# Optimization experiments

Measured on AMD Instinct MI355X. Metric: run time of the kernel, lower is better.

Reference implementation:

```python
import jax, jax.numpy as jnp
import numpy as np

B, D, H, NB = 16384, 1024, 256, 16

def setup_inputs() -> dict:
    key = jax.random.key(0)
    ks = jax.random.split(key, 10)
    s_d = 1.0 / np.sqrt(D)
    s_h = 1.0 / np.sqrt(H)
    return {
        "x":   jax.random.normal(ks[0], (B, D), jnp.float32),
        # switch: Linear(D,H) -> relu -> Linear(H, 3*NB)
        "Ws1": jax.random.normal(ks[1], (D, H), jnp.float32) * s_d,
        "bs1": jnp.zeros((H,), jnp.float32),
        "Ws2": jax.random.normal(ks[2], (H, 3 * NB), jnp.float32) * s_h,
        "bs2": jnp.zeros((3 * NB,), jnp.float32),
        # per-branch bottleneck FC operators: D -> H -> D
        "W1":  jax.random.normal(ks[3], (NB, D, H), jnp.float32) * s_d,
        "b1":  jnp.zeros((NB, H), jnp.float32),
        "W2":  jax.random.normal(ks[4], (NB, H, D), jnp.float32) * s_h,
        "b2":  jnp.zeros((NB, D), jnp.float32),
        # noise: uniform for gumbel, normal for reparameterized gaussian
        "u":   jax.random.uniform(ks[5], (B, NB), jnp.float32, 1e-6, 1.0 - 1e-6),
        "eps": jax.random.normal(ks[6], (B, NB), jnp.float32),
    }

def reference(x, Ws1, bs1, Ws2, bs2, W1, b1, W2, b2, u, eps):
    # switch -> control signals, reshaped to (B, 3, NB)
    ctrl = jax.nn.relu(x @ Ws1 + bs1) @ Ws2 + bs2
    ctrl = ctrl.reshape(-1, 3, NB)
    y_logits, z_mean, z_logvar = ctrl[:, 0], ctrl[:, 1], ctrl[:, 2]

    # gumbel-softmax sample (tau = 1)
    g = -jnp.log(-jnp.log(u))
    y = jax.nn.softmax(y_logits + g, axis=-1)          # soft sample (B, NB)
    y_idx = jnp.argmax(y, axis=-1)                     # hard branch per sample

    # gaussian reparameterization
    z = z_mean + jnp.exp(0.5 * z_logvar) * eps         # (B, NB)

    # per-branch bottleneck FC, z of the branch gates the bottleneck
    h = jax.nn.relu(jnp.einsum('bd,ndh->bnh', x, W1) + b1)   # (B, NB, H)
    h = h * z[:, :, None]
    o = jnp.einsum('bnh,nhd->bnd', h, W2) + b2               # (B, NB, D)

    # combine: keep only the branch selected by y_idx
    onehot = jax.nn.one_hot(y_idx, NB, dtype=x.dtype)        # (B, NB)
    out = jnp.einsum('bnd,bn->bd', o, onehot)                # (B, D)

    return (x + out, y_logits, y_idx, y, z_mean, z_logvar, z)
```

## Files before the change

kernel.cpp:

```cpp
#include <hip/hip_runtime.h>
#include <hip/hip_bf16.h>
#include <stdint.h>

#define Bn 16384
#define Dd 1024
#define Hh 256
#define NBk 16

#define O1 ((size_t)Bn*Dd)
#define O2 (O1 + (size_t)Bn*NBk)
#define O3 (O2 + (size_t)Bn)
#define O4 (O3 + (size_t)Bn*NBk)
#define O5 (O4 + (size_t)Bn*NBk)
#define O6 (O5 + (size_t)Bn*NBk)

typedef __attribute__((ext_vector_type(8))) short s16x8;
typedef __attribute__((ext_vector_type(4))) float f32x4;

#define MFMA_BF16(a,b,c) __builtin_amdgcn_mfma_f32_16x16x32_bf16((a),(b),(c),0,0,0)

__device__ __forceinline__ float blo(unsigned v){ return __uint_as_float(v << 16); }
__device__ __forceinline__ float bhi(unsigned v){ return __uint_as_float(v & 0xFFFF0000u); }
__device__ __forceinline__ unsigned short f2b(float f){
  unsigned u = __float_as_uint(f);
// ... 90 lines not shown
                                           unsigned short* __restrict__ hi,
                                           unsigned short* __restrict__ lo)
{
  const int i0 = blockIdx.x * 32, j0 = blockIdx.y * 32;
  __shared__ float T[32][33];
  const int t = threadIdx.x;
  {
    const int ii = t >> 3, jj = (t & 7) * 4;
    float4 v = *(const float4*)&in[(size_t)(i0+ii)*Hh + j0 + jj];
    T[ii][jj] = v.x; T[ii][jj+1] = v.y; T[ii][jj+2] = v.z; T[ii][jj+3] = v.w;
  }
  __syncthreads();
  {
    const int jo = t >> 3, io = (t & 7) * 4;
    ushort4 sh, sl;
    float v0 = T[io+0][jo], v1 = T[io+1][jo], v2 = T[io+2][jo], v3 = T[io+3][jo];
    unsigned short h;
    h = f2b(v0); sh.x = h; sl.x = f2b(v0 - __uint_as_float((unsigned)h << 16));
    h = f2b(v1); sh.y = h; sl.y = f2b(v1 - __uint_as_float((unsigned)h << 16));
    h = f2b(v2); sh.z = h; sl.z = f2b(v2 - __uint_as_float((unsigned)h << 16));
    h = f2b(v3); sh.w = h; sl.w = f2b(v3 - __uint_as_float((unsigned)h << 16));
    *(ushort4*)&hi[(size_t)(j0+jo)*Dd + i0 + io] = sh;
    *(ushort4*)&lo[(size_t)(j0+jo)*Dd + i0 + io] = sl;
  }
}

__global__ __launch_bounds__(256) void kT2(const float* __restrict__ Ws2, float* __restrict__ Ws2T)
{
  const int j = blockIdx.x;
  const int k = threadIdx.x;
  Ws2T[(size_t)j * Hh + k] = Ws2[(size_t)k * 48 + j];
}

__global__ __launch_bounds__(256) void kA1s(const float* __restrict__ x,
    const unsigned short* __restrict__ Whi, const unsigned short* __restrict__ Wlo,
    const float* __restrict__ bs1, float* __restrict__ A1)
{
  __shared__ __align__(16) float Xs[64*64];
  __shared__ __align__(16) unsigned short Bh[128*64];
  __shared__ __align__(16) unsigned short Bl[128*64];

  const int bid = blockIdx.x;
  const int b0 = (bid >> 1) * 64;
  const int cb = bid & 1;
  const int tid = threadIdx.x, l = tid & 63, w = tid >> 6;
  const int wr = w >> 1, wc = w & 1;

  size_t xsrc[4];
  const unsigned short *hsrc[4], *lsrc[4];
  const unsigned short* Hbase = Whi + (size_t)(cb * 128) * Dd;
  const unsigned short* Lbase = Wlo + (size_t)(cb * 128) * Dd;
  #pragma unroll
  for (int t = 0; t < 4; ++t) {
    {
      int row = (w * 4 + t) * 4 + (l >> 4);
      int ga = (l & 15) ^ (row & 7);
      xsrc[t] = (size_t)(b0 + row) * Dd + ga * 4;
    }
    {
      int row = (w * 4 + t) * 8 + (l >> 3);
      int sa = (l & 7) ^ (row & 7);
      hsrc[t] = Hbase + (size_t)row * Dd + sa * 8;
      lsrc[t] = Lbase + (size_t)row * Dd + sa * 8;
    }
  }

  f32x4 acc[2][4];
  #pragma unroll
  for (int a = 0; a < 2; ++a)
    #pragma unroll
    for (int b_ = 0; b_ < 4; ++b_)
      #pragma unroll
      for (int e = 0; e < 4; ++e) acc[a][b_][e] = 0.f;

  for (int kc = 0; kc < 16; ++kc) {
    #pragma unroll
    for (int t = 0; t < 4; ++t) {
      gload16(&x[xsrc[t] + kc * 64], (char*)Xs + (w * 4 + t) * 1024);
      gload16(hsrc[t] + kc * 64, (char*)Bh + (w * 4 + t) * 1024);
      gload16(lsrc[t] + kc * 64, (char*)Bl + (w * 4 + t) * 1024);
    }
    __syncthreads();

    #pragma unroll
    for (int kk = 0; kk < 2; ++kk) {
      s16x8 ahi[2], alo[2], bh[4], bl[4];
      #pragma unroll
      for (int rf = 0; rf < 2; ++rf) {
        const int row = wr * 32 + rf * 16 + (l & 15);
        const int gl = 8 * kk + 2 * (l >> 4);
        const int g0 = gl ^ (row & 7), g1 = (gl + 1) ^ (row & 7);
        f32x4 u0 = *(const f32x4*)((const char*)Xs + row * 256 + g0 * 16);
        f32x4 u1 = *(const f32x4*)((const char*)Xs + row * 256 + g1 * 16);
        split8(u0, u1, ahi[rf], alo[rf]);
      }
      #pragma unroll
      for (int cf = 0; cf < 4; ++cf) {
        const int col = wc * 64 + cf * 16 + (l & 15);
        const int s8 = (4 * kk + (l >> 4)) ^ (col & 7);
        bh[cf] = *(const s16x8*)((const char*)Bh + col * 128 + s8 * 16);
        bl[cf] = *(const s16x8*)((const char*)Bl + col * 128 + s8 * 16);
      }
      #pragma unroll
      for (int rf = 0; rf < 2; ++rf)
        #pragma unroll
        for (int cf = 0; cf < 4; ++cf) {
          acc[rf][cf] = MFMA_BF16(ahi[rf], bh[cf], acc[rf][cf]);
          acc[rf][cf] = MFMA_BF16(ahi[rf], bl[cf], acc[rf][cf]);
          acc[rf][cf] = MFMA_BF16(alo[rf], bh[cf], acc[rf][cf]);
        }
    }
    __syncthreads();
  }

  #pragma unroll
  for (int rf = 0; rf < 2; ++rf)
    #pragma unroll
    for (int cf = 0; cf < 4; ++cf)
      #pragma unroll
      for (int rg = 0; rg < 4; ++rg) {
        const int row = b0 + wr * 32 + rf * 16 + (l >> 4) * 4 + rg;
        const int col = cb * 128 + wc * 64 + cf * 16 + (l & 15);
        A1[(size_t)row * Hh + col] = fmaxf(acc[rf][cf][rg] + bs1[col], 0.f);
      }
}

__global__ __launch_bounds__(256) void kA2(const float* __restrict__ Ws2, const float* __restrict__ bs2,
                                           float* out)
{
  const int b0 = blockIdx.x * 64;
  __shared__ float XS[32][68];
  __shared__ float WC[32][48];
  const int tid = threadIdx.x;
  const int rg = tid >> 4, jg = tid & 15;
  float acc[4][3];
  #pragma unroll
  for (int r = 0; r < 4; ++r) { acc[r][0]=0.f; acc[r][1]=0.f; acc[r][2]=0.f; }
  const float* A1 = out;
  for (int kc = 0; kc < 8; ++kc) {
    const int k0 = kc*32;
    #pragma unroll
    for (int it = 0; it < 2; ++it) {
      int i = tid + 256*it;
      int row = i >> 3, kq = i & 7;
      float4 v = *(const float4*)&A1[(size_t)(b0+row)*Hh + k0 + 4*kq];
      XS[4*kq+0][row]=v.x; XS[4*kq+1][row]=v.y; XS[4*kq+2][row]=v.z; XS[4*kq+3][row]=v.w;
    }
    #pragma unroll
    for (int it = 0; it < 2; ++it) {
      int i = tid + 256*it;
      if (i < 384) {
        int k = i / 12, jq = i % 12;
        *(float4*)&WC[k][4*jq] = *(const float4*)&Ws2[(size_t)(k0+k)*48 + 4*jq];
      }
    }
    __syncthreads();
    #pragma unroll
// ... 287 lines not shown
        f32x4 u0 = *(const f32x4*)((const char*)Xs + row * 256 + g0 * 16);
        f32x4 u1 = *(const f32x4*)((const char*)Xs + row * 256 + g1 * 16);
        af[rf] = cvt8(u0, u1);
      }
      #pragma unroll
      for (int cf = 0; cf < 4; ++cf) {
        const int col = wc * 64 + cf * 16 + (l & 15);
        const int s8 = (4 * kk + (l >> 4)) ^ (col & 7);
        bf[cf] = *(const s16x8*)((const char*)Wsh + col * 128 + s8 * 16);
      }
      #pragma unroll
      for (int rf = 0; rf < 2; ++rf)
        #pragma unroll
        for (int cf = 0; cf < 4; ++cf)
          acc[rf][cf] = MFMA_BF16(af[rf], bf[cf], acc[rf][cf]);
    }
    __syncthreads();
  }

  const size_t hrow0 = (size_t)seg[n] + r0;
  #pragma unroll
  for (int rf = 0; rf < 2; ++rf)
    #pragma unroll
    for (int cf = 0; cf < 4; ++cf)
      #pragma unroll
      for (int rg = 0; rg < 4; ++rg) {
        const int rloc = wr * 32 + rf * 16 + (l >> 4) * 4 + rg;
        const int col = cb * 128 + wc * 64 + cf * 16 + (l & 15);
        const float hv = fmaxf(acc[rf][cf][rg] + b1[n * Hh + col], 0.f) * zrs[rloc];
        hbuf[(hrow0 + rloc) * Hh + col] = f2b(hv);
      }
}

__global__ __launch_bounds__(256) void kG2(const float* __restrict__ x,
    const unsigned short* __restrict__ W2T, const float* __restrict__ b2,
    const unsigned short* __restrict__ hbuf, const int* __restrict__ rowlist,
    const int* __restrict__ offs, const int* __restrict__ tp2, const int* __restrict__ seg,
    float* __restrict__ out)
{
  __shared__ __align__(16) unsigned short As[128*64];
  __shared__ __align__(16) unsigned short Bs[128*64];
  __shared__ int rows_s[128];

  const int bid = blockIdx.x;
  const int tile = bid >> 3, cb = bid & 7;
  if (tile >= tp2[NBk]) return;
  int n = 0;
  while (tile >= tp2[n+1]) ++n;
  const int tt = tile - tp2[n];
  const int base = offs[n], cnt = offs[n+1] - base;
  const int r0 = tt * 128;
  const int tid = threadIdx.x, l = tid & 63, w = tid >> 6;
  const int wr = w >> 1, wc = w & 1;

  if (tid < 128) {
    int r = r0 + tid;
    rows_s[tid] = rowlist[base + (r < cnt ? r : cnt - 1)];
  }
  __syncthreads();

  const unsigned short* Abase = hbuf + (size_t)(seg[n] + r0) * Hh;
  const unsigned short* Bbase = W2T + (size_t)n * (Hh * Dd) + (size_t)(cb * 128) * Hh;

  const unsigned short* asrc[4];
  const unsigned short* bsrc[4];
  #pragma unroll
// ... 28 lines not shown
        const int row = wr * 64 + rf * 16 + (l & 15);
        const int s8 = (4 * kk + (l >> 4)) ^ (row & 7);
        af[rf] = *(const s16x8*)((const char*)As + row * 128 + s8 * 16);
      }
      #pragma unroll
      for (int cf = 0; cf < 4; ++cf) {
        const int col = wc * 64 + cf * 16 + (l & 15);
        const int s8 = (4 * kk + (l >> 4)) ^ (col & 7);
        bf[cf] = *(const s16x8*)((const char*)Bs + col * 128 + s8 * 16);
      }
      #pragma unroll
      for (int rf = 0; rf < 4; ++rf)
        #pragma unroll
        for (int cf = 0; cf < 4; ++cf)
          acc[rf][cf] = MFMA_BF16(af[rf], bf[cf], acc[rf][cf]);
    }
    __syncthreads();
  }

  #pragma unroll
  for (int rf = 0; rf < 4; ++rf)
    #pragma unroll
    for (int rg = 0; rg < 4; ++rg) {
      const int rloc = wr * 64 + rf * 16 + (l >> 4) * 4 + rg;
      if (r0 + rloc < cnt) {
        const int g = rows_s[rloc];
        #pragma unroll
        for (int cf = 0; cf < 4; ++cf) {
          const int col = cb * 128 + wc * 64 + cf * 16 + (l & 15);
          out[(size_t)g * Dd + col] = acc[rf][cf][rg] + b2[n * Dd + col] + x[(size_t)g * Dd + col];
        }
      }
    }
}

__global__ __launch_bounds__(256) void kCm(const float* __restrict__ x,
    const unsigned short* __restrict__ W1T, const float* __restrict__ b1,
    const unsigned short* __restrict__ W2T, const float* __restrict__ b2,
    const int* __restrict__ rowlist, const float* __restrict__ zsel,
    const int* __restrict__ offs, float* __restrict__ out)
{
  __shared__ __align__(16) char LDSA[55808];
  char* HSp  = LDSA;
  char* XSp  = LDSA + 33792;
  char* W1Sp = LDSA + 33792 + 4096;
  char* W2Sp = LDSA + 33792;
  float* b1s = (float*)(LDSA + 54272);
  int*   rows = (int*)(LDSA + 55296);
  float* zrs  = (float*)(LDSA + 55552);

  const int tid = threadIdx.x;
  const int l = tid & 63, w = tid >> 6;
  const int xcd = blockIdx.x & 7, slot0 = blockIdx.x >> 3;
  const int n0 = 2 * xcd;
  const int oA = offs[n0], oB = offs[n0+1], oC = offs[n0+2];
  const int cA = oB - oA, cB = oC - oB;
  const int nb0 = (cA + 63) >> 6, nb1 = (cB + 63) >> 6;

  const int sr = tid >> 2, sq = tid & 3;

  for (int si = slot0; si < nb0 + nb1; si += 64) {
    int n, base, cnt, tt;
    if (si < nb0) { n = n0;     tt = si;        base = oA; cnt = cA; }
    else          { n = n0 + 1; tt = si - nb0;  base = oB; cnt = cB; }
    const int r0 = tt * 64;

    __syncthreads();
    if (tid < 64) {
      int r = r0 + tid;
      int g = rowlist[base + (r < cnt ? r : cnt - 1)];
      rows[tid] = g;
      zrs[tid]  = zsel[g];
    }
    b1s[tid] = b1[n * Hh + tid];
    __syncthreads();

    const size_t xrow = (size_t)rows[sr] * Dd;
    const size_t w1o = (size_t)n * (Dd * Hh);
    const size_t w2o = (size_t)n * (Hh * Dd);

    f32x4 acc1[4][4];
    #pragma unroll
    for (int a = 0; a < 4; ++a)
      #pragma unroll
      for (int b_ = 0; b_ < 4; ++b_)
        #pragma unroll
        for (int e = 0; e < 4; ++e) acc1[a][b_][e] = 0.f;

    const int arow  = (l & 15) * 64 + (l >> 4) * 16;
    const int brow1 = w * 4096 + (l & 15) * 64 + (l >> 4) * 16;

    float4 xa, xb; uint4 wv0, wv1, wv2, wv3;
    xa = *(const float4*)&x[xrow + sq * 8];
    xb = *(const float4*)&x[xrow + sq * 8 + 4];
    wv0 = *(const uint4*)&W1T[w1o + (size_t)(  0 + sr) * Dd + sq * 8];
    wv1 = *(const uint4*)&W1T[w1o + (size_t)( 64 + sr) * Dd + sq * 8];
    wv2 = *(const uint4*)&W1T[w1o + (size_t)(128 + sr) * Dd + sq * 8];
    wv3 = *(const uint4*)&W1T[w1o + (size_t)(192 + sr) * Dd + sq * 8];
    {
      s16x8 xs;
      xs[0]=(short)f2b(xa.x); xs[1]=(short)f2b(xa.y); xs[2]=(short)f2b(xa.z); xs[3]=(short)f2b(xa.w);
      xs[4]=(short)f2b(xb.x); xs[5]=(short)f2b(xb.y); xs[6]=(short)f2b(xb.z); xs[7]=(short)f2b(xb.w);
      *(s16x8*)(XSp + 16 * tid) = xs;
      *(uint4*)(W1Sp +     0 + 16 * tid) = wv0;
      *(uint4*)(W1Sp +  4096 + 16 * tid) = wv1;
      *(uint4*)(W1Sp +  8192 + 16 * tid) = wv2;
      *(uint4*)(W1Sp + 12288 + 16 * tid) = wv3;
    }
    __syncthreads();

    for (int kc = 0; kc < 32; ++kc) {
      const bool more = kc < 31;
      if (more) {
        const int ko = (kc + 1) * 32 + sq * 8;
        xa = *(const float4*)&x[xrow + ko];
        xb = *(const float4*)&x[xrow + ko + 4];
        wv0 = *(const uint4*)&W1T[w1o + (size_t)(  0 + sr) * Dd + ko];
        wv1 = *(const uint4*)&W1T[w1o + (size_t)( 64 + sr) * Dd + ko];
        wv2 = *(const uint4*)&W1T[w1o + (size_t)(128 + sr) * Dd + ko];
        wv3 = *(const uint4*)&W1T[w1o + (size_t)(192 + sr) * Dd + ko];
      }
      s16x8 af[4], bf[4];
      #pragma unroll
      for (int rt = 0; rt < 4; ++rt) af[rt] = *(const s16x8*)(XSp + rt * 1024 + arow);
      #pragma unroll
      for (int ct = 0; ct < 4; ++ct) bf[ct] = *(const s16x8*)(W1Sp + brow1 + ct * 1024);
      #pragma unroll
      for (int rt = 0; rt < 4; ++rt)
        #pragma unroll
        for (int ct = 0; ct < 4; ++ct)
          acc1[rt][ct] = MFMA_BF16(af[rt], bf[ct], acc1[rt][ct]);
      __syncthreads();
      if (more) {
        s16x8 xs;
        xs[0]=(short)f2b(xa.x); xs[1]=(short)f2b(xa.y); xs[2]=(short)f2b(xa.z); xs[3]=(short)f2b(xa.w);
        xs[4]=(short)f2b(xb.x); xs[5]=(short)f2b(xb.y); xs[6]=(short)f2b(xb.z); xs[7]=(short)f2b(xb.w);
        *(s16x8*)(XSp + 16 * tid) = xs;
        *(uint4*)(W1Sp +     0 + 16 * tid) = wv0;
        *(uint4*)(W1Sp +  4096 + 16 * tid) = wv1;
        *(uint4*)(W1Sp +  8192 + 16 * tid) = wv2;
        *(uint4*)(W1Sp + 12288 + 16 * tid) = wv3;
      }
      __syncthreads();
    }

    #pragma unroll
    for (int rt = 0; rt < 4; ++rt)
      #pragma unroll
      for (int ct = 0; ct < 4; ++ct)
        #pragma unroll
        for (int rg = 0; rg < 4; ++rg) {
          const int row = rt * 16 + 4 * (l >> 4) + rg;
          const int col = w * 64 + ct * 16 + (l & 15);
          const float hv = fmaxf(acc1[rt][ct][rg] + b1s[col], 0.f) * zrs[row];
          *(unsigned short*)(HSp + row * 528 + col * 2) = f2b(hv);
        }
    __syncthreads();

    uint4 v0, v1, v2, v3;
    v0 = *(const uint4*)&W2T[w2o + (size_t)(  0 + sr) * Hh + sq * 8];
    v1 = *(const uint4*)&W2T[w2o + (size_t)( 64 + sr) * Hh + sq * 8];
    v2 = *(const uint4*)&W2T[w2o + (size_t)(128 + sr) * Hh + sq * 8];
    v3 = *(const uint4*)&W2T[w2o + (size_t)(192 + sr) * Hh + sq * 8];
    *(uint4*)(W2Sp +     0 + 16 * tid) = v0;
    *(uint4*)(W2Sp +  4096 + 16 * tid) = v1;
    *(uint4*)(W2Sp +  8192 + 16 * tid) = v2;
    *(uint4*)(W2Sp + 12288 + 16 * tid) = v3;
    __syncthreads();

    for (int s = 0; s < 4; ++s) {
      f32x4 acc2[4][4];
      #pragma unroll
      for (int a = 0; a < 4; ++a)
        #pragma unroll
        for (int b_ = 0; b_ < 4; ++b_)
          #pragma unroll
          for (int e = 0; e < 4; ++e) acc2[a][b_][e] = 0.f;

      for (int kc = 0; kc < 8; ++kc) {
        int ns = s, nk = kc + 1;
        if (nk == 8) { ns = s + 1; nk = 0; }
        const bool more = ns < 4;
        if (more) {
          const size_t dbase = w2o + (size_t)(ns * 256) * Hh;
          const int ko = nk * 32 + sq * 8;
          v0 = *(const uint4*)&W2T[dbase + (size_t)(  0 + sr) * Hh + ko];
          v1 = *(const uint4*)&W2T[dbase + (size_t)( 64 + sr) * Hh + ko];
          v2 = *(const uint4*)&W2T[dbase + (size_t)(128 + sr) * Hh + ko];
          v3 = *(const uint4*)&W2T[dbase + (size_t)(192 + sr) * Hh + ko];
        }
        s16x8 af[4], bf[4];
        #pragma unroll
        for (int rt = 0; rt < 4; ++rt)
          af[rt] = *(const s16x8*)(HSp + (rt * 16 + (l & 15)) * 528 + kc * 64 + (l >> 4) * 16);
        #pragma unroll
        for (int ct = 0; ct < 4; ++ct)
          bf[ct] = *(const s16x8*)(W2Sp + (w * 64 + ct * 16 + (l & 15)) * 64 + (l >> 4) * 16);
        #pragma unroll
        for (int rt = 0; rt < 4; ++rt)
          #pragma unroll
          for (int ct = 0; ct < 4; ++ct)
            acc2[rt][ct] = MFMA_BF16(af[rt], bf[ct], acc2[rt][ct]);
        __syncthreads();
        if (more) {
          *(uint4*)(W2Sp +     0 + 16 * tid) = v0;
          *(uint4*)(W2Sp +  4096 + 16 * tid) = v1;
          *(uint4*)(W2Sp +  8192 + 16 * tid) = v2;
          *(uint4*)(W2Sp + 12288 + 16 * tid) = v3;
        }
        __syncthreads();
      }

      #pragma unroll
      for (int rt = 0; rt < 4; ++rt)
        #pragma unroll
        for (int ct = 0; ct < 4; ++ct)
          #pragma unroll
          for (int rg = 0; rg < 4; ++rg) {
            const int row = rt * 16 + 4 * (l >> 4) + rg;
            if (r0 + row < cnt) {
              const int g = rows[row];
              const int d = s * 256 + w * 64 + ct * 16 + (l & 15);
              out[(size_t)g * Dd + d] = acc2[rt][ct][rg] + b2[n * Dd + d] + x[(size_t)g * Dd + d];
            }
          }
    }
  }
}

extern "C" void kernel_launch(void* const* d_in, const int* in_sizes, int n_in,
                              void* d_out, int out_size, void* d_ws, size_t ws_size,
                              hipStream_t stream) {
  const float* x   = (const float*)d_in[0];
  const float* Ws1 = (const float*)d_in[1];
  const float* bs1 = (const float*)d_in[2];
  const float* Ws2 = (const float*)d_in[3];
  const float* bs2 = (const float*)d_in[4];
  const float* W1  = (const float*)d_in[5];
  const float* b1  = (const float*)d_in[6];
  const float* W2  = (const float*)d_in[7];
  const float* b2  = (const float*)d_in[8];
  const float* u   = (const float*)d_in[9];
  const float* eps = (const float*)d_in[10];
  float* out = (float*)d_out;

  char* ws = (char*)d_ws;
  int*   counts  = (int*)(ws + 0);
  int*   cursor  = (int*)(ws + 64);
  int*   bpre    = (int*)(ws + 128);
  int*   offs    = (int*)(ws + 256);
  int*   tp1     = (int*)(ws + 384);
  int*   tp2     = (int*)(ws + 512);
  int*   seg     = (int*)(ws + 640);
  int*   idxw    = (int*)(ws + 4096);
  float* zsel    = (float*)(ws + 4096 + 65536);
  int*   rowlist = (int*)(ws + 4096 + 131072);
  float* Ws2T    = (float*)(ws + 786432);
  unsigned short* W1T  = (unsigned short*)(ws + ((size_t)1 << 20));
  unsigned short* W2T  = (unsigned short*)(ws + ((size_t)9 << 20));
  unsigned short* hbuf = (unsigned short*)(ws + ((size_t)17 << 20));
  unsigned short* Whi  = (unsigned short*)(ws + ((size_t)27 << 20));
  unsigned short* Wlo  = (unsigned short*)(ws + ((size_t)27 << 20) + (512<<10));

  const bool f2 = ws_size >= ((size_t)28 << 20);
  const bool f1 = ws_size >= ((size_t)18 << 20);

  hipMemsetAsync(d_ws, 0, 4096, stream);
  if (f1 || f2) {
    kT<<<dim3(32, 8, 16), 256, 0, stream>>>(W1, W1T, Dd, Hh);
    kT<<<dim3(8, 32, 16), 256, 0, stream>>>(W2, W2T, Hh, Dd);
  }
  if (f2) {
    kTW<<<dim3(32, 8), 256, 0, stream>>>(Ws1, Whi, Wlo);
    kT2<<<dim3(48), 256, 0, stream>>>(Ws2, Ws2T);
    kA1s<<<dim3(512), 256, 0, stream>>>(x, Whi, Wlo, bs1, out);
    kB3<<<dim3(Bn/16), 256, 0, stream>>>(out, Ws2T, bs2, u, eps, out, idxw, zsel);
    kH <<<dim3(Bn/256), 256, 0, stream>>>(idxw, counts);
  } else {
    kA1<<<dim3(Bn/64, 2), 256, 0, stream>>>(x, Ws1, bs1, out);
    kA2<<<dim3(Bn/64), 256, 0, stream>>>(Ws2, bs2, out);
    kB2<<<dim3(Bn*NBk/256), 256, 0, stream>>>(u, eps, out, idxw, zsel, counts);
  }
  kP <<<dim3(1), 64, 0, stream>>>(counts, offs, cursor, bpre, tp1, tp2, seg);
  if (f2) {
    kS2<<<dim3(Bn/256), 256, 0, stream>>>(idxw, cursor, rowlist);
    kG1<<<dim3(544), 256, 0, stream>>>(x, W1T, b1, rowlist, zsel, offs, tp1, seg, hbuf);
    kG2<<<dim3(1152), 256, 0, stream>>>(x, W2T, b2, hbuf, rowlist, offs, tp2, seg, out);
  } else {
    kS<<<dim3(Bn/256), 256, 0, stream>>>(idxw, cursor, rowlist);
    if (f1)
      kCm<<<dim3(512), 256, 0, stream>>>(x, W1T, b1, W2T, b2, rowlist, zsel, offs, out);
  }
}
```

Measured before the change: 159.7 us.

## Pre-split x into bf16 hi/lo once and reuse in switch and branch GEMMs

Adds a pass that converts x into bf16 high and low halves in workspace. A new switch GEMM kernel reads these directly through async global-to-LDS loads with swizzled layout and smaller 64x64 tiles. A new first branch GEMM reads the bf16 high part instead of fp32 x. This is meant to remove repeated fp32-to-bf16 conversion and halve x traffic inside both GEMMs, at the cost of an extra 64MB write plus reads and a 92MB workspace requirement. The unused fused kCm fallback is removed, so the smallest workspace path no longer computes the branch output.

```diff
diff --git a/kernel.cpp b/kernel.cpp
--- a/kernel.cpp
+++ b/kernel.cpp
@@ -146,6 +146,19 @@
   Ws2T[(size_t)j * Hh + k] = Ws2[(size_t)k * 48 + j];
 }
 
+__global__ __launch_bounds__(256) void kTX(const float* __restrict__ x,
+                                           unsigned short* __restrict__ xh,
+                                           unsigned short* __restrict__ xl)
+{
+  const size_t i = ((size_t)blockIdx.x * 256 + threadIdx.x) * 8;
+  const f32x4 u0 = *(const f32x4*)&x[i];
+  const f32x4 u1 = *(const f32x4*)&x[i + 4];
+  s16x8 hi, lo;
+  split8(u0, u1, hi, lo);
+  *(s16x8*)&xh[i] = hi;
+  *(s16x8*)&xl[i] = lo;
+}
+
 __global__ __launch_bounds__(256) void kA1s(const float* __restrict__ x,
     const unsigned short* __restrict__ Whi, const unsigned short* __restrict__ Wlo,
     const float* __restrict__ bs1, float* __restrict__ A1)
@@ -237,6 +250,86 @@
         const int col = cb * 128 + wc * 64 + cf * 16 + (l & 15);
         A1[(size_t)row * Hh + col] = fmaxf(acc[rf][cf][rg] + bs1[col], 0.f);
       }
+}
+
+__global__ __launch_bounds__(256) void kA1s2(const unsigned short* __restrict__ Xhi,
+    const unsigned short* __restrict__ Xlo,
+    const unsigned short* __restrict__ Whi, const unsigned short* __restrict__ Wlo,
+    const float* __restrict__ bs1, float* __restrict__ A1)
+{
+  __shared__ __align__(16) unsigned short Xh[64*64];
+  __shared__ __align__(16) unsigned short Xl[64*64];
+  __shared__ __align__(16) unsigned short Bh[64*64];
+  __shared__ __align__(16) unsigned short Bl[64*64];
+
+  const int bid = blockIdx.x;
+  const int b0 = (bid >> 2) * 64;
+  const int cb = bid & 3;
+  const int tid = threadIdx.x, l = tid & 63, w = tid >> 6;
+
+  const unsigned short *xhs[2], *xls[2], *whs[2], *wls[2];
+  int ldst[2];
+  const unsigned short* Hbase = Whi + (size_t)(cb * 64) * Dd;
+  const unsigned short* Lbase = Wlo + (size_t)(cb * 64) * Dd;
+  #pragma unroll
+  for (int t = 0; t < 2; ++t) {
+    const int row = (w * 2 + t) * 8 + (l >> 3);
+    const int sa = (l & 7) ^ (row & 7);
+    xhs[t] = Xhi + (size_t)(b0 + row) * Dd + sa * 8;
+    xls[t] = Xlo + (size_t)(b0 + row) * Dd + sa * 8;
+    whs[t] = Hbase + (size_t)row * Dd + sa * 8;
+    wls[t] = Lbase + (size_t)row * Dd + sa * 8;
+    ldst[t] = (w * 2 + t) * 1024;
+  }
+
+  f32x4 acc[4];
+  #pragma unroll
+  for (int cf = 0; cf < 4; ++cf)
+    #pragma unroll
+    for (int e = 0; e < 4; ++e) acc[cf][e] = 0.f;
+
+  for (int kc = 0; kc < 16; ++kc) {
+    #pragma unroll
+    for (int t = 0; t < 2; ++t) {
+      gload16(xhs[t] + kc * 64, (char*)Xh + ldst[t]);
+      gload16(xls[t] + kc * 64, (char*)Xl + ldst[t]);
+      gload16(whs[t] + kc * 64, (char*)Bh + ldst[t]);
+      gload16(wls[t] + kc * 64, (char*)Bl + ldst[t]);
+    }
+    __syncthreads();
+
+    #pragma unroll
+    for (int kk = 0; kk < 2; ++kk) {
+      const int arow = w * 16 + (l & 15);
+      const int as8 = (4 * kk + (l >> 4)) ^ (arow & 7);
+      const s16x8 ah = *(const s16x8*)((const char*)Xh + arow * 128 + as8 * 16);
+      const s16x8 al = *(const s16x8*)((const char*)Xl + arow * 128 + as8 * 16);
+      s16x8 bh[4], bl[4];
+      #pragma unroll
+      for (int cf = 0; cf < 4; ++cf) {
+        const int col = cf * 16 + (l & 15);
+        const int s8 = (4 * kk + (l >> 4)) ^ (col & 7);
+        bh[cf] = *(const s16x8*)((const char*)Bh + col * 128 + s8 * 16);
+        bl[cf] = *(const s16x8*)((const char*)Bl + col * 128 + s8 * 16);
+      }
+      #pragma unroll
+      for (int cf = 0; cf < 4; ++cf) {
+        acc[cf] = MFMA_BF16(ah, bh[cf], acc[cf]);
+        acc[cf] = MFMA_BF16(ah, bl[cf], acc[cf]);
+        acc[cf] = MFMA_BF16(al, bh[cf], acc[cf]);
+      }
+    }
+    __syncthreads();
+  }
+
+  #pragma unroll
+  for (int cf = 0; cf < 4; ++cf)
+    #pragma unroll
+    for (int rg = 0; rg < 4; ++rg) {
+      const int row = b0 + w * 16 + (l >> 4) * 4 + rg;
+      const int col = cb * 64 + cf * 16 + (l & 15);
+      A1[(size_t)row * Hh + col] = fmaxf(acc[cf][rg] + bs1[col], 0.f);
+    }
 }
 
 __global__ __launch_bounds__(256) void kA2(const float* __restrict__ Ws2, const float* __restrict__ bs2,
@@ -590,6 +683,109 @@
       }
 }
 
+__global__ __launch_bounds__(256) void kG1b(const unsigned short* __restrict__ Xhi,
+    const unsigned short* __restrict__ W1T, const float* __restrict__ b1,
+    const int* __restrict__ rowlist, const float* __restrict__ zsel,
+    const int* __restrict__ offs, const int* __restrict__ tp1, const int* __restrict__ seg,
+    unsigned short* __restrict__ hbuf)
+{
+  __shared__ __align__(16) unsigned short Xsh[64*64];
+  __shared__ __align__(16) unsigned short Wsh[128*64];
+  __shared__ int rows_s[64];
+  __shared__ float zrs[64];
+
+  const int bid = blockIdx.x;
+  const int tile = bid >> 1, cb = bid & 1;
+  if (tile >= tp1[NBk]) return;
+  int n = 0;
+  while (tile >= tp1[n+1]) ++n;
+  const int tt = tile - tp1[n];
+  const int base = offs[n], cnt = offs[n+1] - base;
+  const int r0 = tt * 64;
+  const int tid = threadIdx.x, l = tid & 63, w = tid >> 6;
+  const int wr = w >> 1, wc = w & 1;
+
+  if (tid < 64) {
+    int r = r0 + tid;
+    int g = rowlist[base + (r < cnt ? r : cnt - 1)];
+    rows_s[tid] = g;
+    zrs[tid] = zsel[g];
+  }
+  __syncthreads();
+
+  const unsigned short* xsrc[2];
+  int xdst[2];
+  const unsigned short* wsrc[4];
+  const unsigned short* Wbase = W1T + (size_t)n * (Hh * Dd) + (size_t)(cb * 128) * Dd;
+  #pragma unroll
+  for (int t = 0; t < 2; ++t) {
+    const int row = (w * 2 + t) * 8 + (l >> 3);
+    const int sa = (l & 7) ^ (row & 7);
+    xsrc[t] = Xhi + (size_t)rows_s[row] * Dd + sa * 8;
+    xdst[t] = (w * 2 + t) * 1024;
+  }
+  #pragma unroll
+  for (int t = 0; t < 4; ++t) {
+    const int row = (w * 4 + t) * 8 + (l >> 3);
+    const int sa = (l & 7) ^ (row & 7);
+    wsrc[t] = Wbase + (size_t)row * Dd + sa * 8;
+  }
+
+  f32x4 acc[2][4];
+  #pragma unroll
+  for (int a = 0; a < 2; ++a)
+    #pragma unroll
+    for (int b_ = 0; b_ < 4; ++b_)
+      #pragma unroll
+      for (int e = 0; e < 4; ++e) acc[a][b_][e] = 0.f;
+
+  for (int kc = 0; kc < 16; ++kc) {
+    #pragma unroll
+    for (int t = 0; t < 2; ++t)
+      gload16(xsrc[t] + kc * 64, (char*)Xsh + xdst[t]);
+    #pragma unroll
+    for (int t = 0; t < 4; ++t)
+      gload16(wsrc[t] + kc * 64, (char*)Wsh + (w * 4 + t) * 1024);
+    __syncthreads();
+
+    #pragma unroll
+    for (int kk = 0; kk < 2; ++kk) {
+      s16x8 af[2], bf[4];
+      #pragma unroll
+      for (int rf = 0; rf < 2; ++rf) {
+        const int row = wr * 32 + rf * 16 + (l & 15);
+        const int s8 = (4 * kk + (l >> 4)) ^ (row & 7);
+        af[rf] = *(const s16x8*)((const char*)Xsh + row * 128 + s8 * 16);
+      }
+      #pragma unroll
+      for (int cf = 0; cf < 4; ++cf) {
+        const int col = wc * 64 + cf * 16 + (l & 15);
+        const int s8 = (4 * kk + (l >> 4)) ^ (col & 7);
+        bf[cf] = *(const s16x8*)((const char*)Wsh + col * 128 + s8 * 16);
+      }
+      #pragma unroll
+      for (int rf = 0; rf < 2; ++rf)
+        #pragma unroll
+        for (int cf = 0; cf < 4; ++cf)
+          acc[rf][cf] = MFMA_BF16(af[rf], bf[cf], acc[rf][cf]);
+    }
+    __syncthreads();
+  }
+
+  const size_t hrow0 = (size_t)seg[n] + r0;
+  #pragma unroll
+  for (int rf = 0; rf < 2; ++rf)
+    #pragma unroll
+    for (int cf = 0; cf < 4; ++cf)
+      #pragma unroll
+      for (int rg = 0; rg < 4; ++rg) {
+        const int rloc = wr * 32 + rf * 16 + (l >> 4) * 4 + rg;
+        const int col = cb * 128 + wc * 64 + cf * 16 + (l & 15);
+        const float hv = fmaxf(acc[rf][cf][rg] + b1[n * Hh + col], 0.f) * zrs[rloc];
+        hbuf[(hrow0 + rloc) * Hh + col] = f2b(hv);
+      }
+}
+
 __global__ __launch_bounds__(256) void kG2(const float* __restrict__ x,
     const unsigned short* __restrict__ W2T, const float* __restrict__ b2,
     const unsigned short* __restrict__ hbuf, const int* __restrict__ rowlist,
@@ -684,200 +880,6 @@
         }
       }
     }
-}
-
-__global__ __launch_bounds__(256) void kCm(const float* __restrict__ x,
-    const unsigned short* __restrict__ W1T, const float* __restrict__ b1,
-    const unsigned short* __restrict__ W2T, const float* __restrict__ b2,
-    const int* __restrict__ rowlist, const float* __restrict__ zsel,
-    const int* __restrict__ offs, float* __restrict__ out)
-{
-  __shared__ __align__(16) char LDSA[55808];
-  char* HSp  = LDSA;
-  char* XSp  = LDSA + 33792;
-  char* W1Sp = LDSA + 33792 + 4096;
-  char* W2Sp = LDSA + 33792;
-  float* b1s = (float*)(LDSA + 54272);
-  int*   rows = (int*)(LDSA + 55296);
-  float* zrs  = (float*)(LDSA + 55552);
-
-  const int tid = threadIdx.x;
-  const int l = tid & 63, w = tid >> 6;
-  const int xcd = blockIdx.x & 7, slot0 = blockIdx.x >> 3;
-  const int n0 = 2 * xcd;
-  const int oA = offs[n0], oB = offs[n0+1], oC = offs[n0+2];
-  const int cA = oB - oA, cB = oC - oB;
-  const int nb0 = (cA + 63) >> 6, nb1 = (cB + 63) >> 6;
-
-  const int sr = tid >> 2, sq = tid & 3;
-
-  for (int si = slot0; si < nb0 + nb1; si += 64) {
-    int n, base, cnt, tt;
-    if (si < nb0) { n = n0;     tt = si;        base = oA; cnt = cA; }
-    else          { n = n0 + 1; tt = si - nb0;  base = oB; cnt = cB; }
-    const int r0 = tt * 64;
-
-    __syncthreads();
-    if (tid < 64) {
-      int r = r0 + tid;
-      int g = rowlist[base + (r < cnt ? r : cnt - 1)];
-      rows[tid] = g;
-      zrs[tid]  = zsel[g];
-    }
-    b1s[tid] = b1[n * Hh + tid];
-    __syncthreads();
-
-    const size_t xrow = (size_t)rows[sr] * Dd;
-    const size_t w1o = (size_t)n * (Dd * Hh);
-    const size_t w2o = (size_t)n * (Hh * Dd);
-
-    f32x4 acc1[4][4];
-    #pragma unroll
-    for (int a = 0; a < 4; ++a)
-      #pragma unroll
-      for (int b_ = 0; b_ < 4; ++b_)
-        #pragma unroll
-        for (int e = 0; e < 4; ++e) acc1[a][b_][e] = 0.f;
-
-    const int arow  = (l & 15) * 64 + (l >> 4) * 16;
-    const int brow1 = w * 4096 + (l & 15) * 64 + (l >> 4) * 16;
-
-    float4 xa, xb; uint4 wv0, wv1, wv2, wv3;
-    xa = *(const float4*)&x[xrow + sq * 8];
-    xb = *(const float4*)&x[xrow + sq * 8 + 4];
-    wv0 = *(const uint4*)&W1T[w1o + (size_t)(  0 + sr) * Dd + sq * 8];
-    wv1 = *(const uint4*)&W1T[w1o + (size_t)( 64 + sr) * Dd + sq * 8];
-    wv2 = *(const uint4*)&W1T[w1o + (size_t)(128 + sr) * Dd + sq * 8];
-    wv3 = *(const uint4*)&W1T[w1o + (size_t)(192 + sr) * Dd + sq * 8];
-    {
-      s16x8 xs;
-      xs[0]=(short)f2b(xa.x); xs[1]=(short)f2b(xa.y); xs[2]=(short)f2b(xa.z); xs[3]=(short)f2b(xa.w);
-      xs[4]=(short)f2b(xb.x); xs[5]=(short)f2b(xb.y); xs[6]=(short)f2b(xb.z); xs[7]=(short)f2b(xb.w);
-      *(s16x8*)(XSp + 16 * tid) = xs;
-      *(uint4*)(W1Sp +     0 + 16 * tid) = wv0;
-      *(uint4*)(W1Sp +  4096 + 16 * tid) = wv1;
-      *(uint4*)(W1Sp +  8192 + 16 * tid) = wv2;
-      *(uint4*)(W1Sp + 12288 + 16 * tid) = wv3;
-    }
-    __syncthreads();
-
-    for (int kc = 0; kc < 32; ++kc) {
-      const bool more = kc < 31;
-      if (more) {
-        const int ko = (kc + 1) * 32 + sq * 8;
-        xa = *(const float4*)&x[xrow + ko];
-        xb = *(const float4*)&x[xrow + ko + 4];
-        wv0 = *(const uint4*)&W1T[w1o + (size_t)(  0 + sr) * Dd + ko];
-        wv1 = *(const uint4*)&W1T[w1o + (size_t)( 64 + sr) * Dd + ko];
-        wv2 = *(const uint4*)&W1T[w1o + (size_t)(128 + sr) * Dd + ko];
-        wv3 = *(const uint4*)&W1T[w1o + (size_t)(192 + sr) * Dd + ko];
-      }
-      s16x8 af[4], bf[4];
-      #pragma unroll
-      for (int rt = 0; rt < 4; ++rt) af[rt] = *(const s16x8*)(XSp + rt * 1024 + arow);
-      #pragma unroll
-      for (int ct = 0; ct < 4; ++ct) bf[ct] = *(const s16x8*)(W1Sp + brow1 + ct * 1024);
-      #pragma unroll
-      for (int rt = 0; rt < 4; ++rt)
-        #pragma unroll
-        for (int ct = 0; ct < 4; ++ct)
-          acc1[rt][ct] = MFMA_BF16(af[rt], bf[ct], acc1[rt][ct]);
-      __syncthreads();
-      if (more) {
-        s16x8 xs;
-        xs[0]=(short)f2b(xa.x); xs[1]=(short)f2b(xa.y); xs[2]=(short)f2b(xa.z); xs[3]=(short)f2b(xa.w);
-        xs[4]=(short)f2b(xb.x); xs[5]=(short)f2b(xb.y); xs[6]=(short)f2b(xb.z); xs[7]=(short)f2b(xb.w);
-        *(s16x8*)(XSp + 16 * tid) = xs;
-        *(uint4*)(W1Sp +     0 + 16 * tid) = wv0;
-        *(uint4*)(W1Sp +  4096 + 16 * tid) = wv1;
-        *(uint4*)(W1Sp +  8192 + 16 * tid) = wv2;
-        *(uint4*)(W1Sp + 12288 + 16 * tid) = wv3;
-      }
-      __syncthreads();
-    }
-
-    #pragma unroll
-    for (int rt = 0; rt < 4; ++rt)
-      #pragma unroll
-      for (int ct = 0; ct < 4; ++ct)
-        #pragma unroll
-        for (int rg = 0; rg < 4; ++rg) {
-          const int row = rt * 16 + 4 * (l >> 4) + rg;
-          const int col = w * 64 + ct * 16 + (l & 15);
-          const float hv = fmaxf(acc1[rt][ct][rg] + b1s[col], 0.f) * zrs[row];
-          *(unsigned short*)(HSp + row * 528 + col * 2) = f2b(hv);
-        }
-    __syncthreads();
-
-    uint4 v0, v1, v2, v3;
-    v0 = *(const uint4*)&W2T[w2o + (size_t)(  0 + sr) * Hh + sq * 8];
-    v1 = *(const uint4*)&W2T[w2o + (size_t)( 64 + sr) * Hh + sq * 8];
-    v2 = *(const uint4*)&W2T[w2o + (size_t)(128 + sr) * Hh + sq * 8];
-    v3 = *(const uint4*)&W2T[w2o + (size_t)(192 + sr) * Hh + sq * 8];
-    *(uint4*)(W2Sp +     0 + 16 * tid) = v0;
-    *(uint4*)(W2Sp +  4096 + 16 * tid) = v1;
-    *(uint4*)(W2Sp +  8192 + 16 * tid) = v2;
-    *(uint4*)(W2Sp + 12288 + 16 * tid) = v3;
-    __syncthreads();
-
-    for (int s = 0; s < 4; ++s) {
-      f32x4 acc2[4][4];
-      #pragma unroll
-      for (int a = 0; a < 4; ++a)
-        #pragma unroll
-        for (int b_ = 0; b_ < 4; ++b_)
-          #pragma unroll
-          for (int e = 0; e < 4; ++e) acc2[a][b_][e] = 0.f;
-
-      for (int kc = 0; kc < 8; ++kc) {
-        int ns = s, nk = kc + 1;
-        if (nk == 8) { ns = s + 1; nk = 0; }
-        const bool more = ns < 4;
-        if (more) {
-          const size_t dbase = w2o + (size_t)(ns * 256) * Hh;
-          const int ko = nk * 32 + sq * 8;
-          v0 = *(const uint4*)&W2T[dbase + (size_t)(  0 + sr) * Hh + ko];
-          v1 = *(const uint4*)&W2T[dbase + (size_t)( 64 + sr) * Hh + ko];
-          v2 = *(const uint4*)&W2T[dbase + (size_t)(128 + sr) * Hh + ko];
-          v3 = *(const uint4*)&W2T[dbase + (size_t)(192 + sr) * Hh + ko];
-        }
-        s16x8 af[4], bf[4];
-        #pragma unroll
-        for (int rt = 0; rt < 4; ++rt)
-          af[rt] = *(const s16x8*)(HSp + (rt * 16 + (l & 15)) * 528 + kc * 64 + (l >> 4) * 16);
-        #pragma unroll
-        for (int ct = 0; ct < 4; ++ct)
-          bf[ct] = *(const s16x8*)(W2Sp + (w * 64 + ct * 16 + (l & 15)) * 64 + (l >> 4) * 16);
-        #pragma unroll
-        for (int rt = 0; rt < 4; ++rt)
-          #pragma unroll
-          for (int ct = 0; ct < 4; ++ct)
-            acc2[rt][ct] = MFMA_BF16(af[rt], bf[ct], acc2[rt][ct]);
-        __syncthreads();
-        if (more) {
-          *(uint4*)(W2Sp +     0 + 16 * tid) = v0;
-          *(uint4*)(W2Sp +  4096 + 16 * tid) = v1;
-          *(uint4*)(W2Sp +  8192 + 16 * tid) = v2;
-          *(uint4*)(W2Sp + 12288 + 16 * tid) = v3;
-        }
-        __syncthreads();
-      }
-
-      #pragma unroll
-      for (int rt = 0; rt < 4; ++rt)
-        #pragma unroll
-        for (int ct = 0; ct < 4; ++ct)
-          #pragma unroll
-          for (int rg = 0; rg < 4; ++rg) {
-            const int row = rt * 16 + 4 * (l >> 4) + rg;
-            if (r0 + row < cnt) {
-              const int g = rows[row];
-              const int d = s * 256 + w * 64 + ct * 16 + (l & 15);
-              out[(size_t)g * Dd + d] = acc2[rt][ct][rg] + b2[n * Dd + d] + x[(size_t)g * Dd + d];
-            }
-          }
-    }
-  }
 }
 
 extern "C" void kernel_launch(void* const* d_in, const int* in_sizes, int n_in,
@@ -913,7 +915,10 @@
   unsigned short* hbuf = (unsigned short*)(ws + ((size_t)17 << 20));
   unsigned short* Whi  = (unsigned short*)(ws + ((size_t)27 << 20));
   unsigned short* Wlo  = (unsigned short*)(ws + ((size_t)27 << 20) + (512<<10));
-
+  unsigned short* Xhi  = (unsigned short*)(ws + ((size_t)28 << 20));
+  unsigned short* Xlo  = (unsigned short*)(ws + ((size_t)60 << 20));
+
+  const bool f3 = ws_size >= ((size_t)92 << 20);
   const bool f2 = ws_size >= ((size_t)28 << 20);
   const bool f1 = ws_size >= ((size_t)18 << 20);
 
@@ -925,7 +930,12 @@
   if (f2) {
     kTW<<<dim3(32, 8), 256, 0, stream>>>(Ws1, Whi, Wlo);
     kT2<<<dim3(48), 256, 0, stream>>>(Ws2, Ws2T);
-    kA1s<<<dim3(512), 256, 0, stream>>>(x, Whi, Wlo, bs1, out);
+    if (f3) {
+      kTX<<<dim3(Bn*Dd/2048), 256, 0, stream>>>(x, Xhi, Xlo);
+      kA1s2<<<dim3(1024), 256, 0, stream>>>(Xhi, Xlo, Whi, Wlo, bs1, out);
+    } else {
+      kA1s<<<dim3(512), 256, 0, stream>>>(x, Whi, Wlo, bs1, out);
+    }
     kB3<<<dim3(Bn/16), 256, 0, stream>>>(out, Ws2T, bs2, u, eps, out, idxw, zsel);
     kH <<<dim3(Bn/256), 256, 0, stream>>>(idxw, counts);
   } else {
@@ -936,11 +946,12 @@
   kP <<<dim3(1), 64, 0, stream>>>(counts, offs, cursor, bpre, tp1, tp2, seg);
   if (f2) {
     kS2<<<dim3(Bn/256), 256, 0, stream>>>(idxw, cursor, rowlist);
-    kG1<<<dim3(544), 256, 0, stream>>>(x, W1T, b1, rowlist, zsel, offs, tp1, seg, hbuf);
+    if (f3)
+      kG1b<<<dim3(544), 256, 0, stream>>>(Xhi, W1T, b1, rowlist, zsel, offs, tp1, seg, hbuf);
+    else
+      kG1<<<dim3(544), 256, 0, stream>>>(x, W1T, b1, rowlist, zsel, offs, tp1, seg, hbuf);
     kG2<<<dim3(1152), 256, 0, stream>>>(x, W2T, b2, hbuf, rowlist, offs, tp2, seg, out);
   } else {
     kS<<<dim3(Bn/256), 256, 0, stream>>>(idxw, cursor, rowlist);
-    if (f1)
-      kCm<<<dim3(512), 256, 0, stream>>>(x, W1T, b1, W2T, b2, rowlist, zsel, offs, out);
-  }
-}
+  }
+}
```

New measurement: 173.5 us. 1.09x slower.

## Split x into bf16 hi/lo once per tile in first switch GEMM, halve row tile

Applied to the files above, without the earlier changes.

The first switch GEMM kernel now converts each x element to bf16 hi/lo once when it is staged into shared memory, and stores it as bf16. Before, every wave re-split fp32 tiles on each fragment read. The row tile drops from 64 to 32 rows, each wave covers 32 columns instead of a 2x4 fragment grid, and the grid doubles to 1024 blocks. The x load for the next k-chunk is register-prefetched while MFMAs run on the current chunk. The unused fallback kernel kCm is removed, so the small-workspace path no longer computes the branch output, though that path does not run normally.

```diff
diff --git a/kernel.cpp b/kernel.cpp
--- a/kernel.cpp
+++ b/kernel.cpp
@@ -146,82 +146,89 @@
   Ws2T[(size_t)j * Hh + k] = Ws2[(size_t)k * 48 + j];
 }
 
-__global__ __launch_bounds__(256) void kA1s(const float* __restrict__ x,
+__global__ __launch_bounds__(256) void kA1s3(const float* __restrict__ x,
     const unsigned short* __restrict__ Whi, const unsigned short* __restrict__ Wlo,
     const float* __restrict__ bs1, float* __restrict__ A1)
 {
-  __shared__ __align__(16) float Xs[64*64];
+  __shared__ __align__(16) unsigned short Xh[32*64];
+  __shared__ __align__(16) unsigned short Xl[32*64];
   __shared__ __align__(16) unsigned short Bh[128*64];
   __shared__ __align__(16) unsigned short Bl[128*64];
 
   const int bid = blockIdx.x;
-  const int b0 = (bid >> 1) * 64;
+  const int b0 = (bid >> 1) * 32;
   const int cb = bid & 1;
   const int tid = threadIdx.x, l = tid & 63, w = tid >> 6;
-  const int wr = w >> 1, wc = w & 1;
-
-  size_t xsrc[4];
+
+  const int xrow = tid >> 3, xga = tid & 7;
+  const int xdst = xrow * 128 + (xga ^ (xrow & 7)) * 16;
+  const size_t xsrc = (size_t)(b0 + xrow) * Dd + xga * 8;
+
   const unsigned short *hsrc[4], *lsrc[4];
   const unsigned short* Hbase = Whi + (size_t)(cb * 128) * Dd;
   const unsigned short* Lbase = Wlo + (size_t)(cb * 128) * Dd;
   #pragma unroll
   for (int t = 0; t < 4; ++t) {
-    {
-      int row = (w * 4 + t) * 4 + (l >> 4);
-      int ga = (l & 15) ^ (row & 7);
-      xsrc[t] = (size_t)(b0 + row) * Dd + ga * 4;
-    }
-    {
-      int row = (w * 4 + t) * 8 + (l >> 3);
-      int sa = (l & 7) ^ (row & 7);
-      hsrc[t] = Hbase + (size_t)row * Dd + sa * 8;
-      lsrc[t] = Lbase + (size_t)row * Dd + sa * 8;
-    }
-  }
-
-  f32x4 acc[2][4];
+    const int col = (w * 4 + t) * 8 + (l >> 3);
+    const int sa = (l & 7) ^ (col & 7);
+    hsrc[t] = Hbase + (size_t)col * Dd + sa * 8;
+    lsrc[t] = Lbase + (size_t)col * Dd + sa * 8;
+  }
+
+  f32x4 acc[2][2];
   #pragma unroll
   for (int a = 0; a < 2; ++a)
     #pragma unroll
-    for (int b_ = 0; b_ < 4; ++b_)
+    for (int b_ = 0; b_ < 2; ++b_)
       #pragma unroll
       for (int e = 0; e < 4; ++e) acc[a][b_][e] = 0.f;
 
+  f32x4 xa = *(const f32x4*)&x[xsrc];
+  f32x4 xb = *(const f32x4*)&x[xsrc + 4];
+
   for (int kc = 0; kc < 16; ++kc) {
     #pragma unroll
     for (int t = 0; t < 4; ++t) {
-      gload16(&x[xsrc[t] + kc * 64], (char*)Xs + (w * 4 + t) * 1024);
       gload16(hsrc[t] + kc * 64, (char*)Bh + (w * 4 + t) * 1024);
       gload16(lsrc[t] + kc * 64, (char*)Bl + (w * 4 + t) * 1024);
     }
-    __syncthreads();
+    {
+      s16x8 hi8, lo8;
+      split8(xa, xb, hi8, lo8);
+      *(s16x8*)((char*)Xh + xdst) = hi8;
+      *(s16x8*)((char*)Xl + xdst) = lo8;
+    }
+    __syncthreads();
+
+    if (kc < 15) {
+      xa = *(const f32x4*)&x[xsrc + (kc + 1) * 64];
+      xb = *(const f32x4*)&x[xsrc + (kc + 1) * 64 + 4];
+    }
 
     #pragma unroll
     for (int kk = 0; kk < 2; ++kk) {
-      s16x8 ahi[2], alo[2], bh[4], bl[4];
+      s16x8 ah[2], al[2], bh[2], bl[2];
       #pragma unroll
       for (int rf = 0; rf < 2; ++rf) {
-        const int row = wr * 32 + rf * 16 + (l & 15);
-        const int gl = 8 * kk + 2 * (l >> 4);
-        const int g0 = gl ^ (row & 7), g1 = (gl + 1) ^ (row & 7);
-        f32x4 u0 = *(const f32x4*)((const char*)Xs + row * 256 + g0 * 16);
-        f32x4 u1 = *(const f32x4*)((const char*)Xs + row * 256 + g1 * 16);
-        split8(u0, u1, ahi[rf], alo[rf]);
-      }
-      #pragma unroll
-      for (int cf = 0; cf < 4; ++cf) {
-        const int col = wc * 64 + cf * 16 + (l & 15);
-        const int s8 = (4 * kk + (l >> 4)) ^ (col & 7);
-        bh[cf] = *(const s16x8*)((const char*)Bh + col * 128 + s8 * 16);
-        bl[cf] = *(const s16x8*)((const char*)Bl + col * 128 + s8 * 16);
+        const int row = rf * 16 + (l & 15);
+        const int g = (kk * 4 + (l >> 4)) ^ (row & 7);
+        ah[rf] = *(const s16x8*)((const char*)Xh + row * 128 + g * 16);
+        al[rf] = *(const s16x8*)((const char*)Xl + row * 128 + g * 16);
+      }
+      #pragma unroll
+      for (int cf = 0; cf < 2; ++cf) {
+        const int col = w * 32 + cf * 16 + (l & 15);
+        const int g = (kk * 4 + (l >> 4)) ^ (col & 7);
+        bh[cf] = *(const s16x8*)((const char*)Bh + col * 128 + g * 16);
+        bl[cf] = *(const s16x8*)((const char*)Bl + col * 128 + g * 16);
       }
       #pragma unroll
       for (int rf = 0; rf < 2; ++rf)
         #pragma unroll
-        for (int cf = 0; cf < 4; ++cf) {
-          acc[rf][cf] = MFMA_BF16(ahi[rf], bh[cf], acc[rf][cf]);
-          acc[rf][cf] = MFMA_BF16(ahi[rf], bl[cf], acc[rf][cf]);
-          acc[rf][cf] = MFMA_BF16(alo[rf], bh[cf], acc[rf][cf]);
+        for (int cf = 0; cf < 2; ++cf) {
+          acc[rf][cf] = MFMA_BF16(ah[rf], bh[cf], acc[rf][cf]);
+          acc[rf][cf] = MFMA_BF16(ah[rf], bl[cf], acc[rf][cf]);
+          acc[rf][cf] = MFMA_BF16(al[rf], bh[cf], acc[rf][cf]);
         }
     }
     __syncthreads();
@@ -230,11 +237,11 @@
   #pragma unroll
   for (int rf = 0; rf < 2; ++rf)
     #pragma unroll
-    for (int cf = 0; cf < 4; ++cf)
+    for (int cf = 0; cf < 2; ++cf)
       #pragma unroll
       for (int rg = 0; rg < 4; ++rg) {
-        const int row = b0 + wr * 32 + rf * 16 + (l >> 4) * 4 + rg;
-        const int col = cb * 128 + wc * 64 + cf * 16 + (l & 15);
+        const int row = b0 + rf * 16 + (l >> 4) * 4 + rg;
+        const int col = cb * 128 + w * 32 + cf * 16 + (l & 15);
         A1[(size_t)row * Hh + col] = fmaxf(acc[rf][cf][rg] + bs1[col], 0.f);
       }
 }
@@ -684,200 +691,6 @@
         }
       }
     }
-}
-
-__global__ __launch_bounds__(256) void kCm(const float* __restrict__ x,
-    const unsigned short* __restrict__ W1T, const float* __restrict__ b1,
-    const unsigned short* __restrict__ W2T, const float* __restrict__ b2,
-    const int* __restrict__ rowlist, const float* __restrict__ zsel,
-    const int* __restrict__ offs, float* __restrict__ out)
-{
-  __shared__ __align__(16) char LDSA[55808];
-  char* HSp  = LDSA;
-  char* XSp  = LDSA + 33792;
-  char* W1Sp = LDSA + 33792 + 4096;
-  char* W2Sp = LDSA + 33792;
-  float* b1s = (float*)(LDSA + 54272);
-  int*   rows = (int*)(LDSA + 55296);
-  float* zrs  = (float*)(LDSA + 55552);
-
-  const int tid = threadIdx.x;
-  const int l = tid & 63, w = tid >> 6;
-  const int xcd = blockIdx.x & 7, slot0 = blockIdx.x >> 3;
-  const int n0 = 2 * xcd;
-  const int oA = offs[n0], oB = offs[n0+1], oC = offs[n0+2];
-  const int cA = oB - oA, cB = oC - oB;
-  const int nb0 = (cA + 63) >> 6, nb1 = (cB + 63) >> 6;
-
-  const int sr = tid >> 2, sq = tid & 3;
-
-  for (int si = slot0; si < nb0 + nb1; si += 64) {
-    int n, base, cnt, tt;
-    if (si < nb0) { n = n0;     tt = si;        base = oA; cnt = cA; }
-    else          { n = n0 + 1; tt = si - nb0;  base = oB; cnt = cB; }
-    const int r0 = tt * 64;
-
-    __syncthreads();
-    if (tid < 64) {
-      int r = r0 + tid;
-      int g = rowlist[base + (r < cnt ? r : cnt - 1)];
-      rows[tid] = g;
-      zrs[tid]  = zsel[g];
-    }
-    b1s[tid] = b1[n * Hh + tid];
-    __syncthreads();
-
-    const size_t xrow = (size_t)rows[sr] * Dd;
-    const size_t w1o = (size_t)n * (Dd * Hh);
-    const size_t w2o = (size_t)n * (Hh * Dd);
-
-    f32x4 acc1[4][4];
-    #pragma unroll
-    for (int a = 0; a < 4; ++a)
-      #pragma unroll
-      for (int b_ = 0; b_ < 4; ++b_)
-        #pragma unroll
-        for (int e = 0; e < 4; ++e) acc1[a][b_][e] = 0.f;
-
-    const int arow  = (l & 15) * 64 + (l >> 4) * 16;
-    const int brow1 = w * 4096 + (l & 15) * 64 + (l >> 4) * 16;
-
-    float4 xa, xb; uint4 wv0, wv1, wv2, wv3;
-    xa = *(const float4*)&x[xrow + sq * 8];
-    xb = *(const float4*)&x[xrow + sq * 8 + 4];
-    wv0 = *(const uint4*)&W1T[w1o + (size_t)(  0 + sr) * Dd + sq * 8];
-    wv1 = *(const uint4*)&W1T[w1o + (size_t)( 64 + sr) * Dd + sq * 8];
-    wv2 = *(const uint4*)&W1T[w1o + (size_t)(128 + sr) * Dd + sq * 8];
-    wv3 = *(const uint4*)&W1T[w1o + (size_t)(192 + sr) * Dd + sq * 8];
-    {
-      s16x8 xs;
-      xs[0]=(short)f2b(xa.x); xs[1]=(short)f2b(xa.y); xs[2]=(short)f2b(xa.z); xs[3]=(short)f2b(xa.w);
-      xs[4]=(short)f2b(xb.x); xs[5]=(short)f2b(xb.y); xs[6]=(short)f2b(xb.z); xs[7]=(short)f2b(xb.w);
-      *(s16x8*)(XSp + 16 * tid) = xs;
-      *(uint4*)(W1Sp +     0 + 16 * tid) = wv0;
-      *(uint4*)(W1Sp +  4096 + 16 * tid) = wv1;
-      *(uint4*)(W1Sp +  8192 + 16 * tid) = wv2;
-      *(uint4*)(W1Sp + 12288 + 16 * tid) = wv3;
-    }
-    __syncthreads();
-
-    for (int kc = 0; kc < 32; ++kc) {
-      const bool more = kc < 31;
-      if (more) {
-        const int ko = (kc + 1) * 32 + sq * 8;
-        xa = *(const float4*)&x[xrow + ko];
-        xb = *(const float4*)&x[xrow + ko + 4];
-        wv0 = *(const uint4*)&W1T[w1o + (size_t)(  0 + sr) * Dd + ko];
-        wv1 = *(const uint4*)&W1T[w1o + (size_t)( 64 + sr) * Dd + ko];
-        wv2 = *(const uint4*)&W1T[w1o + (size_t)(128 + sr) * Dd + ko];
-        wv3 = *(const uint4*)&W1T[w1o + (size_t)(192 + sr) * Dd + ko];
-      }
-      s16x8 af[4], bf[4];
-      #pragma unroll
-      for (int rt = 0; rt < 4; ++rt) af[rt] = *(const s16x8*)(XSp + rt * 1024 + arow);
-      #pragma unroll
-      for (int ct = 0; ct < 4; ++ct) bf[ct] = *(const s16x8*)(W1Sp + brow1 + ct * 1024);
-      #pragma unroll
-      for (int rt = 0; rt < 4; ++rt)
-        #pragma unroll
-        for (int ct = 0; ct < 4; ++ct)
-          acc1[rt][ct] = MFMA_BF16(af[rt], bf[ct], acc1[rt][ct]);
-      __syncthreads();
-      if (more) {
-        s16x8 xs;
-        xs[0]=(short)f2b(xa.x); xs[1]=(short)f2b(xa.y); xs[2]=(short)f2b(xa.z); xs[3]=(short)f2b(xa.w);
-        xs[4]=(short)f2b(xb.x); xs[5]=(short)f2b(xb.y); xs[6]=(short)f2b(xb.z); xs[7]=(short)f2b(xb.w);
-        *(s16x8*)(XSp + 16 * tid) = xs;
-        *(uint4*)(W1Sp +     0 + 16 * tid) = wv0;
-        *(uint4*)(W1Sp +  4096 + 16 * tid) = wv1;
-        *(uint4*)(W1Sp +  8192 + 16 * tid) = wv2;
-        *(uint4*)(W1Sp + 12288 + 16 * tid) = wv3;
-      }
-      __syncthreads();
-    }
-
-    #pragma unroll
-    for (int rt = 0; rt < 4; ++rt)
-      #pragma unroll
-      for (int ct = 0; ct < 4; ++ct)
-        #pragma unroll
-        for (int rg = 0; rg < 4; ++rg) {
-          const int row = rt * 16 + 4 * (l >> 4) + rg;
-          const int col = w * 64 + ct * 16 + (l & 15);
-          const float hv = fmaxf(acc1[rt][ct][rg] + b1s[col], 0.f) * zrs[row];
-          *(unsigned short*)(HSp + row * 528 + col * 2) = f2b(hv);
-        }
-    __syncthreads();
-
-    uint4 v0, v1, v2, v3;
-    v0 = *(const uint4*)&W2T[w2o + (size_t)(  0 + sr) * Hh + sq * 8];
-    v1 = *(const uint4*)&W2T[w2o + (size_t)( 64 + sr) * Hh + sq * 8];
-    v2 = *(const uint4*)&W2T[w2o + (size_t)(128 + sr) * Hh + sq * 8];
-    v3 = *(const uint4*)&W2T[w2o + (size_t)(192 + sr) * Hh + sq * 8];
-    *(uint4*)(W2Sp +     0 + 16 * tid) = v0;
-    *(uint4*)(W2Sp +  4096 + 16 * tid) = v1;
-    *(uint4*)(W2Sp +  8192 + 16 * tid) = v2;
-    *(uint4*)(W2Sp + 12288 + 16 * tid) = v3;
-    __syncthreads();
-
-    for (int s = 0; s < 4; ++s) {
-      f32x4 acc2[4][4];
-      #pragma unroll
-      for (int a = 0; a < 4; ++a)
-        #pragma unroll
-        for (int b_ = 0; b_ < 4; ++b_)
-          #pragma unroll
-          for (int e = 0; e < 4; ++e) acc2[a][b_][e] = 0.f;
-
-      for (int kc = 0; kc < 8; ++kc) {
-        int ns = s, nk = kc + 1;
-        if (nk == 8) { ns = s + 1; nk = 0; }
-        const bool more = ns < 4;
-        if (more) {
-          const size_t dbase = w2o + (size_t)(ns * 256) * Hh;
-          const int ko = nk * 32 + sq * 8;
-          v0 = *(const uint4*)&W2T[dbase + (size_t)(  0 + sr) * Hh + ko];
-          v1 = *(const uint4*)&W2T[dbase + (size_t)( 64 + sr) * Hh + ko];
-          v2 = *(const uint4*)&W2T[dbase + (size_t)(128 + sr) * Hh + ko];
-          v3 = *(const uint4*)&W2T[dbase + (size_t)(192 + sr) * Hh + ko];
-        }
-        s16x8 af[4], bf[4];
-        #pragma unroll
-        for (int rt = 0; rt < 4; ++rt)
-          af[rt] = *(const s16x8*)(HSp + (rt * 16 + (l & 15)) * 528 + kc * 64 + (l >> 4) * 16);
-        #pragma unroll
-        for (int ct = 0; ct < 4; ++ct)
-          bf[ct] = *(const s16x8*)(W2Sp + (w * 64 + ct * 16 + (l & 15)) * 64 + (l >> 4) * 16);
-        #pragma unroll
-        for (int rt = 0; rt < 4; ++rt)
-          #pragma unroll
-          for (int ct = 0; ct < 4; ++ct)
-            acc2[rt][ct] = MFMA_BF16(af[rt], bf[ct], acc2[rt][ct]);
-        __syncthreads();
-        if (more) {
-          *(uint4*)(W2Sp +     0 + 16 * tid) = v0;
-          *(uint4*)(W2Sp +  4096 + 16 * tid) = v1;
-          *(uint4*)(W2Sp +  8192 + 16 * tid) = v2;
-          *(uint4*)(W2Sp + 12288 + 16 * tid) = v3;
-        }
-        __syncthreads();
-      }
-
-      #pragma unroll
-      for (int rt = 0; rt < 4; ++rt)
-        #pragma unroll
-        for (int ct = 0; ct < 4; ++ct)
-          #pragma unroll
-          for (int rg = 0; rg < 4; ++rg) {
-            const int row = rt * 16 + 4 * (l >> 4) + rg;
-            if (r0 + row < cnt) {
-              const int g = rows[row];
-              const int d = s * 256 + w * 64 + ct * 16 + (l & 15);
-              out[(size_t)g * Dd + d] = acc2[rt][ct][rg] + b2[n * Dd + d] + x[(size_t)g * Dd + d];
-            }
-          }
-    }
-  }
 }
 
 extern "C" void kernel_launch(void* const* d_in, const int* in_sizes, int n_in,
@@ -925,7 +738,7 @@
   if (f2) {
     kTW<<<dim3(32, 8), 256, 0, stream>>>(Ws1, Whi, Wlo);
     kT2<<<dim3(48), 256, 0, stream>>>(Ws2, Ws2T);
-    kA1s<<<dim3(512), 256, 0, stream>>>(x, Whi, Wlo, bs1, out);
+    kA1s3<<<dim3(1024), 256, 0, stream>>>(x, Whi, Wlo, bs1, out);
     kB3<<<dim3(Bn/16), 256, 0, stream>>>(out, Ws2T, bs2, u, eps, out, idxw, zsel);
     kH <<<dim3(Bn/256), 256, 0, stream>>>(idxw, counts);
   } else {
@@ -940,7 +753,5 @@
     kG2<<<dim3(1152), 256, 0, stream>>>(x, W2T, b2, hbuf, rowlist, offs, tp2, seg, out);
   } else {
     kS<<<dim3(Bn/256), 256, 0, stream>>>(idxw, cursor, rowlist);
-    if (f1)
-      kCm<<<dim3(512), 256, 0, stream>>>(x, W1T, b1, W2T, b2, rowlist, zsel, offs, out);
-  }
-}
+  }
+}
```

New measurement: 160.1 us. No clear change (+0.2%).
